# Performance work log

Measured on AMD Instinct MI355X. Metric: run time of the kernel, lower is better.

Reference implementation:

```python
import jax, jax.numpy as jnp
import numpy as np

B, D, R, E, L = 16384, 1024, 64, 4, 3


def setup_inputs() -> dict:
    key = jax.random.key(0)
    ks = jax.random.split(key, 6)
    x0 = jax.random.normal(ks[0], (B, D), dtype=jnp.float32)
    # Expert low-rank factors: U projects D->R, V projects R->D (both bias-free)
    U = jax.random.normal(ks[1], (L, E, D, R), dtype=jnp.float32) * (1.0 / np.sqrt(D))
    V = jax.random.normal(ks[2], (L, E, R, D), dtype=jnp.float32) * (1.0 / np.sqrt(R))
    # Gate Linear(D, E) with bias
    gW = jax.random.normal(ks[3], (L, D, E), dtype=jnp.float32) * (1.0 / np.sqrt(D))
    gb = jax.random.normal(ks[4], (L, E), dtype=jnp.float32) * 0.01
    # Per-layer bias added after mixing (initialized zeros in torch; small random here)
    bias = jax.random.normal(ks[5], (L, D), dtype=jnp.float32) * 0.01
    return {"x0": x0, "U": U, "V": V, "gW": gW, "gb": gb, "bias": bias}


def reference(x0, U, V, gW, gb, bias):
    x = x0
    for l in range(L):
        # batched low-rank expert MLPs: [B,D] -> [B,E,R] -> relu -> [B,E,D]
        h = jax.nn.relu(jnp.einsum('bd,edr->ber', x, U[l]))
        expert_out = jnp.einsum('ber,erd->bed', h, V[l])
        # soft gate over experts
        gate = jax.nn.softmax(x @ gW[l] + gb[l], axis=-1)  # [B,E]
        mixed = jnp.einsum('be,bed->bd', gate, expert_out)  # [B,D]
        x = x0 * mixed + bias[l] + x
    return x
```

## Files before the change

kernel.cpp:

```cpp
#include <hip/hip_runtime.h>

#define DEVI __device__ __forceinline__

typedef __bf16 bf16x8 __attribute__((ext_vector_type(8)));
typedef float f32x4 __attribute__((ext_vector_type(4)));
typedef unsigned short u16x8 __attribute__((ext_vector_type(8)));

DEVI unsigned short f2bf(float f) {
  unsigned u = __builtin_bit_cast(unsigned, f);
  u += 0x7FFFu + ((u >> 16) & 1u);
  return (unsigned short)(u >> 16);
}
DEVI float bf2f(unsigned short h) {
  return __builtin_bit_cast(float, (unsigned)h << 16);
}


__global__ __launch_bounds__(256) void cast_x0_kernel(const float* __restrict__ x,
                                                      unsigned short* __restrict__ xb) {
  int i = blockIdx.x * 256 + threadIdx.x;
  const f32x4* p = (const f32x4*)x;
  f32x4 a = p[2 * i], b = p[2 * i + 1];
  u16x8 o;
  o[0] = f2bf(a[0]); o[1] = f2bf(a[1]); o[2] = f2bf(a[2]); o[3] = f2bf(a[3]);
  o[4] = f2bf(b[0]); o[5] = f2bf(b[1]); o[6] = f2bf(b[2]); o[7] = f2bf(b[3]);
  ((u16x8*)xb)[i] = o;
}

__global__ __launch_bounds__(256) void pack_w1_kernel(const float* __restrict__ U,
                                                      unsigned short* __restrict__ W1T) {
  int idx = blockIdx.x * 256 + threadIdx.x;
  int l = idx >> 18;
  int rem = idx & 262143;
  int n = rem >> 10, k = rem & 1023;
  int e = n >> 6, r = n & 63;
  W1T[idx] = f2bf(U[(size_t)(((l * 4 + e) << 10) + k) * 64 + r]);
}

__global__ __launch_bounds__(256) void pack_v2_kernel(const float* __restrict__ V,
                                                      unsigned short* __restrict__ V2T) {
  int idx = blockIdx.x * 256 + threadIdx.x;
  int l = idx >> 18;
  int rem = idx & 262143;
  int d = rem >> 8, c = rem & 255;
  int e = c >> 6, r = c & 63;
  V2T[idx] = f2bf(V[(size_t)(((l * 4 + e) * 64 + r) << 10) + d]);
}

__global__ __launch_bounds__(256) void pack_gw_kernel(const float* __restrict__ gW,
                                                      unsigned short* __restrict__ gWT) {
  int idx = blockIdx.x * 256 + threadIdx.x;
  int l = idx >> 14;
  int n = (idx >> 10) & 15;
  int k = idx & 1023;
  float v = (n < 4) ? gW[l * 4096 + k * 4 + n] : 0.0f;
  gWT[idx] = f2bf(v);
}

__global__ __launch_bounds__(256) void k1_kernel(const unsigned short* __restrict__ A,
                                                 const unsigned short* __restrict__ Bw,
                                                 const unsigned short* __restrict__ gWT,
                                                 const float* __restrict__ gb,
                                                 unsigned short* __restrict__ Hg) {
  constexpr int K = 1024;
  __shared__ char lds[20480];
  __shared__ float gls[128];
  int t = threadIdx.x;
  int wid = t >> 6, lane = t & 63;
  int g4 = lane >> 4, l15 = lane & 15;
  int wm = wid >> 1, wn = wid & 1;

  int j = blockIdx.x;
  int s = j >> 3;
  int p = (j & 7) * 64 + (s >> 1);
  int ybl = s & 1;
  int m0 = p * 32, n0 = ybl * 128;

  int srow = t >> 3;
  int scolb = ((t & 7) * 16) ^ ((srow & 7) << 4);
  const unsigned short* Asrc = A + (size_t)(m0 + srow) * K + (scolb >> 1);
  const unsigned short* Bsrc = Bw + (size_t)(n0 + srow) * K + (scolb >> 1);

  f32x4 acc[4], accg;
  {
    f32x4 z = {0.f, 0.f, 0.f, 0.f};
    accg = z;
#pragma unroll
    for (int n = 0; n < 4; ++n) acc[n] = z;
  }

  for (int ks = 0; ks < K; ks += 64) {
    __syncthreads();
    __builtin_amdgcn_global_load_lds(
        (const __attribute__((address_space(1))) void*)(Asrc + ks),
        (__attribute__((address_space(3))) void*)(lds + wid * 1024), 16, 0, 0);
#pragma unroll
    for (int i = 0; i < 4; ++i)
      __builtin_amdgcn_global_load_lds(
          (const __attribute__((address_space(1))) void*)(Bsrc + (size_t)i * 32 * K + ks),
          (__attribute__((address_space(3))) void*)(lds + 4096 + i * 4096 + wid * 1024), 16, 0, 0);
    __syncthreads();
#pragma unroll
    for (int kk = 0; kk < 2; ++kk) {
      bf16x8 af;
      {
        int row = wm * 16 + l15;
        af = *(const bf16x8*)(lds + row * 128 + ((kk * 64 + g4 * 16) ^ ((row & 7) << 4)));
      }
      bf16x8 gf;
      if (wn == 0) gf = *(const bf16x8*)(gWT + (size_t)l15 * 1024 + ks + kk * 32 + g4 * 8);
#pragma unroll
      for (int n = 0; n < 4; ++n) {
        int row = wn * 64 + n * 16 + l15;
        bf16x8 bfr = *(const bf16x8*)(lds + 4096 + row * 128 +
                                      ((kk * 64 + g4 * 16) ^ ((row & 7) << 4)));
        acc[n] = __builtin_amdgcn_mfma_f32_16x16x32_bf16(af, bfr, acc[n], 0, 0, 0);
      }
      if (wn == 0)
        accg = __builtin_amdgcn_mfma_f32_16x16x32_bf16(af, gf, accg, 0, 0, 0);
    }
  }

  if (wn == 0) {
    float gbv = gb[l15 & 3];
#pragma unroll
    for (int jj = 0; jj < 4; ++jj) {
      float v = accg[jj] + gbv;
      float mx = fmaxf(v, __shfl_xor(v, 1));
      mx = fmaxf(mx, __shfl_xor(mx, 2));
      float ev = __expf(v - mx);
      float sm = ev + __shfl_xor(ev, 1);
      sm += __shfl_xor(sm, 2);
      if (l15 < 4) gls[(wm * 16 + g4 * 4 + jj) * 4 + l15] = ev / sm;
    }
  }
  __syncthreads();

  int e = ybl * 2 + wn;
#pragma unroll
  for (int n = 0; n < 4; ++n) {
#pragma unroll
    for (int jj = 0; jj < 4; ++jj) {
      int row = wm * 16 + g4 * 4 + jj;
      int col = wn * 64 + n * 16 + l15;
      float v = fmaxf(acc[n][jj], 0.f) * gls[row * 4 + e];
      *(unsigned short*)(lds + 4096 + row * 256 + ((col * 2) ^ ((row & 7) << 4))) = f2bf(v);
    }
  }
  __syncthreads();

#pragma unroll
  for (int i = 0; i < 2; ++i) {
    int row = i * 16 + (t >> 4);
    int seg = (t & 15) * 16;
    u16x8 v = *(const u16x8*)(lds + 4096 + row * 256 + (seg ^ ((row & 7) << 4)));
    *(u16x8*)(Hg + (size_t)(m0 + row) * 256 + n0 + (seg >> 1)) = v;
  }
}

__global__ __launch_bounds__(256) void k2_kernel(const unsigned short* __restrict__ A,
                                                 const unsigned short* __restrict__ Bw,
                                                 const unsigned short* __restrict__ x0b,
                                                 const float* __restrict__ x0f,
                                                 const unsigned short* __restrict__ xcur,
                                                 const float* __restrict__ biasl,
                                                 unsigned short* __restrict__ xnext,
                                                 float* __restrict__ out,
                                                 int last, int use_x0b) {
  constexpr int K = 256;
  __shared__ char lds[24576];
  int t = threadIdx.x;
  int wid = t >> 6, lane = t & 63;
  int g4 = lane >> 4, l15 = lane & 15;
  int wm = wid >> 1, wn = wid & 1;

  int j = blockIdx.x;
  int s = j >> 3;
  int xbl = (j & 7) * 32 + (s >> 3);
  int ybl = s & 7;
  int m0 = xbl * 64, n0 = ybl * 128;

  int srow = t >> 3;
  int scolb = ((t & 7) * 16) ^ ((srow & 7) << 4);
  const unsigned short* Asrc = A + (size_t)(m0 + srow) * K + (scolb >> 1);
  const unsigned short* Bsrc = Bw + (size_t)(n0 + srow) * K + (scolb >> 1);

  f32x4 acc[2][4];
#pragma unroll
  for (int m = 0; m < 2; ++m)
#pragma unroll
    for (int n = 0; n < 4; ++n) { f32x4 z = {0.f, 0.f, 0.f, 0.f}; acc[m][n] = z; }

  for (int ks = 0; ks < K; ks += 64) {
    __syncthreads();
#pragma unroll
    for (int i = 0; i < 2; ++i)
      __builtin_amdgcn_global_load_lds(
          (const __attribute__((address_space(1))) void*)(Asrc + (size_t)i * 32 * K + ks),
          (__attribute__((address_space(3))) void*)(lds + i * 4096 + wid * 1024), 16, 0, 0);
#pragma unroll
    for (int i = 0; i < 4; ++i)
      __builtin_amdgcn_global_load_lds(
          (const __attribute__((address_space(1))) void*)(Bsrc + (size_t)i * 32 * K + ks),
          (__attribute__((address_space(3))) void*)(lds + 8192 + i * 4096 + wid * 1024), 16, 0, 0);
    __syncthreads();
#pragma unroll
    for (int kk = 0; kk < 2; ++kk) {
      bf16x8 af[2];
#pragma unroll
      for (int m = 0; m < 2; ++m) {
        int row = wm * 32 + m * 16 + l15;
        af[m] = *(const bf16x8*)(lds + row * 128 + ((kk * 64 + g4 * 16) ^ ((row & 7) << 4)));
      }
#pragma unroll
      for (int n = 0; n < 4; ++n) {
        int row = wn * 64 + n * 16 + l15;
        bf16x8 bfr = *(const bf16x8*)(lds + 8192 + row * 128 +
                                      ((kk * 64 + g4 * 16) ^ ((row & 7) << 4)));
#pragma unroll
        for (int m = 0; m < 2; ++m)
          acc[m][n] = __builtin_amdgcn_mfma_f32_16x16x32_bf16(af[m], bfr, acc[m][n], 0, 0, 0);
      }
    }
  }
  __syncthreads();

#pragma unroll
  for (int m = 0; m < 2; ++m) {
#pragma unroll
    for (int n = 0; n < 4; ++n) {
#pragma unroll
      for (int jj = 0; jj < 4; ++jj) {
        int row = wm * 32 + m * 16 + g4 * 4 + jj;
        int col = wn * 64 + n * 16 + l15;
        *(unsigned short*)(lds + 8192 + row * 256 + ((col * 2) ^ ((row & 7) << 4))) =
            f2bf(acc[m][n][jj]);
      }
    }
  }
  __syncthreads();

#pragma unroll
  for (int i = 0; i < 4; ++i) {
    int row = i * 16 + (t >> 4);
    int seg = (t & 15) * 16;
    u16x8 a8 = *(const u16x8*)(lds + 8192 + row * 256 + (seg ^ ((row & 7) << 4)));
    size_t goff = (size_t)(m0 + row) * 1024 + n0 + (seg >> 1);
    u16x8 cv = *(const u16x8*)(xcur + goff);
    float x0v[8];
    if (use_x0b) {
      u16x8 xv = *(const u16x8*)(x0b + goff);
#pragma unroll
      for (int k = 0; k < 8; ++k) x0v[k] = bf2f(xv[k]);
    } else {
      f32x4 xa = *(const f32x4*)(x0f + goff);
      f32x4 xb2 = *(const f32x4*)(x0f + goff + 4);
#pragma unroll
      for (int k = 0; k < 4; ++k) { x0v[k] = xa[k]; x0v[k + 4] = xb2[k]; }
    }
    const float* bp = biasl + n0 + (seg >> 1);
    f32x4 b0 = *(const f32x4*)bp;
    f32x4 b1 = *(const f32x4*)(bp + 4);
    float r[8];
#pragma unroll
    for (int k = 0; k < 8; ++k) {
      float bv = (k < 4) ? b0[k & 3] : b1[k & 3];
      r[k] = x0v[k] * bf2f(a8[k]) + bv + bf2f(cv[k]);
    }
    if (last) {
      f32x4 r0, r1;
#pragma unroll
      for (int k = 0; k < 4; ++k) { r0[k] = r[k]; r1[k] = r[k + 4]; }
      *(f32x4*)(out + goff) = r0;
      *(f32x4*)(out + goff + 4) = r1;
    } else {
      u16x8 o;
#pragma unroll
      for (int k = 0; k < 8; ++k) o[k] = f2bf(r[k]);
      *(u16x8*)(xnext + goff) = o;
    }
  }
}

extern "C" void kernel_launch(void* const* d_in, const int* in_sizes, int n_in,
                              void* d_out, int out_size, void* d_ws, size_t ws_size,
                              hipStream_t stream) {
  const float* x0 = (const float*)d_in[0];
  const float* U = (const float*)d_in[1];
  const float* V = (const float*)d_in[2];
  const float* gW = (const float*)d_in[3];
  const float* gb = (const float*)d_in[4];
  const float* bias = (const float*)d_in[5];
  float* out = (float*)d_out;
  char* ws = (char*)d_ws;

  const size_t SZ_X = 33554432;
  const size_t SZ_HG = 8388608;
  const size_t SZ_W = 1572864;
  const size_t SZ_GW = 98304;
  bool use_x0b = ws_size >= (2 * SZ_X + SZ_HG + 2 * SZ_W + SZ_GW);

  size_t off = 0;
  unsigned short* x0b = nullptr;
  if (use_x0b) { x0b = (unsigned short*)(ws + off); off += SZ_X; }
  unsigned short* xbf = (unsigned short*)(ws + off); off += SZ_X;
  unsigned short* hg = (unsigned short*)(ws + off); off += SZ_HG;
  unsigned short* W1T = (unsigned short*)(ws + off); off += SZ_W;
  unsigned short* V2T = (unsigned short*)(ws + off); off += SZ_W;
  unsigned short* gWT = (unsigned short*)(ws + off); off += SZ_GW;

  unsigned short* xinit = use_x0b ? x0b : xbf;

  cast_x0_kernel<<<8192, 256, 0, stream>>>(x0, xinit);
  pack_w1_kernel<<<3072, 256, 0, stream>>>(U, W1T);
  pack_v2_kernel<<<3072, 256, 0, stream>>>(V, V2T);
  pack_gw_kernel<<<192, 256, 0, stream>>>(gW, gWT);

  for (int l = 0; l < 3; ++l) {
    const unsigned short* xs = (l == 0) ? xinit : xbf;
    k1_kernel<<<1024, 256, 0, stream>>>(xs, W1T + l * 262144, gWT + l * 16384,
                                        gb + l * 4, hg);
    k2_kernel<<<2048, 256, 0, stream>>>(hg, V2T + l * 262144,
                                        use_x0b ? x0b : nullptr, x0, xs,
                                        bias + l * 1024, xbf, out,
                                        (l == 2) ? 1 : 0, use_x0b ? 1 : 0);
  }
}
```

Baseline: 178.4 us.

## Double K-step to 128 in both GEMMs and halve k2 M-tile to 32 rows

Both GEMM kernels now stage 128-wide K slices per iteration, which halves the number of barrier-separated load/compute rounds and doubles LDS use to 40 KB. k2 also shrinks its M tile from 64 to 32 rows and doubles its grid to 4096 blocks, giving more blocks but less reuse of each B tile per block. The larger LDS footprint may lower occupancy, and the smaller k2 tile increases total weight traffic from L2.

```diff
diff --git a/kernel.cpp b/kernel.cpp
--- a/kernel.cpp
+++ b/kernel.cpp
@@ -63,7 +63,7 @@
                                                  const float* __restrict__ gb,
                                                  unsigned short* __restrict__ Hg) {
   constexpr int K = 1024;
-  __shared__ char lds[20480];
+  __shared__ char lds[40960];
   __shared__ float gls[128];
   int t = threadIdx.x;
   int wid = t >> 6, lane = t & 63;
@@ -76,8 +76,8 @@
   int ybl = s & 1;
   int m0 = p * 32, n0 = ybl * 128;
 
-  int srow = t >> 3;
-  int scolb = ((t & 7) * 16) ^ ((srow & 7) << 4);
+  int srow = t >> 4;
+  int scolb = ((t & 15) * 16) ^ ((srow & 7) << 4);
   const unsigned short* Asrc = A + (size_t)(m0 + srow) * K + (scolb >> 1);
   const unsigned short* Bsrc = Bw + (size_t)(n0 + srow) * K + (scolb >> 1);
 
@@ -89,31 +89,33 @@
     for (int n = 0; n < 4; ++n) acc[n] = z;
   }
 
-  for (int ks = 0; ks < K; ks += 64) {
+  for (int ks = 0; ks < K; ks += 128) {
     __syncthreads();
-    __builtin_amdgcn_global_load_lds(
-        (const __attribute__((address_space(1))) void*)(Asrc + ks),
-        (__attribute__((address_space(3))) void*)(lds + wid * 1024), 16, 0, 0);
-#pragma unroll
-    for (int i = 0; i < 4; ++i)
+#pragma unroll
+    for (int i = 0; i < 2; ++i)
       __builtin_amdgcn_global_load_lds(
-          (const __attribute__((address_space(1))) void*)(Bsrc + (size_t)i * 32 * K + ks),
-          (__attribute__((address_space(3))) void*)(lds + 4096 + i * 4096 + wid * 1024), 16, 0, 0);
+          (const __attribute__((address_space(1))) void*)(Asrc + (size_t)i * 16 * K + ks),
+          (__attribute__((address_space(3))) void*)(lds + i * 4096 + wid * 1024), 16, 0, 0);
+#pragma unroll
+    for (int i = 0; i < 8; ++i)
+      __builtin_amdgcn_global_load_lds(
+          (const __attribute__((address_space(1))) void*)(Bsrc + (size_t)i * 16 * K + ks),
+          (__attribute__((address_space(3))) void*)(lds + 8192 + i * 4096 + wid * 1024), 16, 0, 0);
     __syncthreads();
 #pragma unroll
-    for (int kk = 0; kk < 2; ++kk) {
+    for (int kk = 0; kk < 4; ++kk) {
+      int kkb = kk * 64 + g4 * 16;
       bf16x8 af;
       {
         int row = wm * 16 + l15;
-        af = *(const bf16x8*)(lds + row * 128 + ((kk * 64 + g4 * 16) ^ ((row & 7) << 4)));
+        af = *(const bf16x8*)(lds + row * 256 + (kkb ^ ((row & 7) << 4)));
       }
       bf16x8 gf;
       if (wn == 0) gf = *(const bf16x8*)(gWT + (size_t)l15 * 1024 + ks + kk * 32 + g4 * 8);
 #pragma unroll
       for (int n = 0; n < 4; ++n) {
         int row = wn * 64 + n * 16 + l15;
-        bf16x8 bfr = *(const bf16x8*)(lds + 4096 + row * 128 +
-                                      ((kk * 64 + g4 * 16) ^ ((row & 7) << 4)));
+        bf16x8 bfr = *(const bf16x8*)(lds + 8192 + row * 256 + (kkb ^ ((row & 7) << 4)));
         acc[n] = __builtin_amdgcn_mfma_f32_16x16x32_bf16(af, bfr, acc[n], 0, 0, 0);
       }
       if (wn == 0)
@@ -144,7 +146,7 @@
       int row = wm * 16 + g4 * 4 + jj;
       int col = wn * 64 + n * 16 + l15;
       float v = fmaxf(acc[n][jj], 0.f) * gls[row * 4 + e];
-      *(unsigned short*)(lds + 4096 + row * 256 + ((col * 2) ^ ((row & 7) << 4))) = f2bf(v);
+      *(unsigned short*)(lds + 8192 + row * 256 + ((col * 2) ^ ((row & 7) << 4))) = f2bf(v);
     }
   }
   __syncthreads();
@@ -153,7 +155,7 @@
   for (int i = 0; i < 2; ++i) {
     int row = i * 16 + (t >> 4);
     int seg = (t & 15) * 16;
-    u16x8 v = *(const u16x8*)(lds + 4096 + row * 256 + (seg ^ ((row & 7) << 4)));
+    u16x8 v = *(const u16x8*)(lds + 8192 + row * 256 + (seg ^ ((row & 7) << 4)));
     *(u16x8*)(Hg + (size_t)(m0 + row) * 256 + n0 + (seg >> 1)) = v;
   }
 }
@@ -168,7 +170,7 @@
                                                  float* __restrict__ out,
                                                  int last, int use_x0b) {
   constexpr int K = 256;
-  __shared__ char lds[24576];
+  __shared__ char lds[40960];
   int t = threadIdx.x;
   int wid = t >> 6, lane = t & 63;
   int g4 = lane >> 4, l15 = lane & 15;
@@ -176,72 +178,64 @@
 
   int j = blockIdx.x;
   int s = j >> 3;
-  int xbl = (j & 7) * 32 + (s >> 3);
+  int xbl = (j & 7) * 64 + (s >> 3);
   int ybl = s & 7;
-  int m0 = xbl * 64, n0 = ybl * 128;
-
-  int srow = t >> 3;
-  int scolb = ((t & 7) * 16) ^ ((srow & 7) << 4);
+  int m0 = xbl * 32, n0 = ybl * 128;
+
+  int srow = t >> 4;
+  int scolb = ((t & 15) * 16) ^ ((srow & 7) << 4);
   const unsigned short* Asrc = A + (size_t)(m0 + srow) * K + (scolb >> 1);
   const unsigned short* Bsrc = Bw + (size_t)(n0 + srow) * K + (scolb >> 1);
 
-  f32x4 acc[2][4];
-#pragma unroll
-  for (int m = 0; m < 2; ++m)
-#pragma unroll
-    for (int n = 0; n < 4; ++n) { f32x4 z = {0.f, 0.f, 0.f, 0.f}; acc[m][n] = z; }
-
-  for (int ks = 0; ks < K; ks += 64) {
+  f32x4 acc[4];
+#pragma unroll
+  for (int n = 0; n < 4; ++n) { f32x4 z = {0.f, 0.f, 0.f, 0.f}; acc[n] = z; }
+
+  for (int ks = 0; ks < K; ks += 128) {
     __syncthreads();
 #pragma unroll
     for (int i = 0; i < 2; ++i)
       __builtin_amdgcn_global_load_lds(
-          (const __attribute__((address_space(1))) void*)(Asrc + (size_t)i * 32 * K + ks),
+          (const __attribute__((address_space(1))) void*)(Asrc + (size_t)i * 16 * K + ks),
           (__attribute__((address_space(3))) void*)(lds + i * 4096 + wid * 1024), 16, 0, 0);
 #pragma unroll
-    for (int i = 0; i < 4; ++i)
+    for (int i = 0; i < 8; ++i)
       __builtin_amdgcn_global_load_lds(
-          (const __attribute__((address_space(1))) void*)(Bsrc + (size_t)i * 32 * K + ks),
+          (const __attribute__((address_space(1))) void*)(Bsrc + (size_t)i * 16 * K + ks),
           (__attribute__((address_space(3))) void*)(lds + 8192 + i * 4096 + wid * 1024), 16, 0, 0);
     __syncthreads();
 #pragma unroll
-    for (int kk = 0; kk < 2; ++kk) {
-      bf16x8 af[2];
-#pragma unroll
-      for (int m = 0; m < 2; ++m) {
-        int row = wm * 32 + m * 16 + l15;
-        af[m] = *(const bf16x8*)(lds + row * 128 + ((kk * 64 + g4 * 16) ^ ((row & 7) << 4)));
+    for (int kk = 0; kk < 4; ++kk) {
+      int kkb = kk * 64 + g4 * 16;
+      bf16x8 af;
+      {
+        int row = wm * 16 + l15;
+        af = *(const bf16x8*)(lds + row * 256 + (kkb ^ ((row & 7) << 4)));
       }
 #pragma unroll
       for (int n = 0; n < 4; ++n) {
         int row = wn * 64 + n * 16 + l15;
-        bf16x8 bfr = *(const bf16x8*)(lds + 8192 + row * 128 +
-                                      ((kk * 64 + g4 * 16) ^ ((row & 7) << 4)));
-#pragma unroll
-        for (int m = 0; m < 2; ++m)
-          acc[m][n] = __builtin_amdgcn_mfma_f32_16x16x32_bf16(af[m], bfr, acc[m][n], 0, 0, 0);
+        bf16x8 bfr = *(const bf16x8*)(lds + 8192 + row * 256 + (kkb ^ ((row & 7) << 4)));
+        acc[n] = __builtin_amdgcn_mfma_f32_16x16x32_bf16(af, bfr, acc[n], 0, 0, 0);
       }
     }
   }
   __syncthreads();
 
 #pragma unroll
-  for (int m = 0; m < 2; ++m) {
-#pragma unroll
-    for (int n = 0; n < 4; ++n) {
-#pragma unroll
-      for (int jj = 0; jj < 4; ++jj) {
-        int row = wm * 32 + m * 16 + g4 * 4 + jj;
-        int col = wn * 64 + n * 16 + l15;
-        *(unsigned short*)(lds + 8192 + row * 256 + ((col * 2) ^ ((row & 7) << 4))) =
-            f2bf(acc[m][n][jj]);
-      }
+  for (int n = 0; n < 4; ++n) {
+#pragma unroll
+    for (int jj = 0; jj < 4; ++jj) {
+      int row = wm * 16 + g4 * 4 + jj;
+      int col = wn * 64 + n * 16 + l15;
+      *(unsigned short*)(lds + 8192 + row * 256 + ((col * 2) ^ ((row & 7) << 4))) =
+          f2bf(acc[n][jj]);
     }
   }
   __syncthreads();
 
 #pragma unroll
-  for (int i = 0; i < 4; ++i) {
+  for (int i = 0; i < 2; ++i) {
     int row = i * 16 + (t >> 4);
     int seg = (t & 15) * 16;
     u16x8 a8 = *(const u16x8*)(lds + 8192 + row * 256 + (seg ^ ((row & 7) << 4)));
@@ -320,7 +314,7 @@
     const unsigned short* xs = (l == 0) ? xinit : xbf;
     k1_kernel<<<1024, 256, 0, stream>>>(xs, W1T + l * 262144, gWT + l * 16384,
                                         gb + l * 4, hg);
-    k2_kernel<<<2048, 256, 0, stream>>>(hg, V2T + l * 262144,
+    k2_kernel<<<4096, 256, 0, stream>>>(hg, V2T + l * 262144,
                                         use_x0b ? x0b : nullptr, x0, xs,
                                         bias + l * 1024, xbf, out,
                                         (l == 2) ? 1 : 0, use_x0b ? 1 : 0);
```

After: 209.0 us. 1.17x slower.

## Double-buffer k1 LDS tiles to overlap global loads with MFMA compute

Applied to the files above, without the earlier changes.

Doubles the k1 kernel's LDS buffer so the next K-slice is fetched with global_load_lds while the current slice feeds the MFMAs. Synchronisation moves from __syncthreads pairs to explicit vmcnt waits plus s_barrier. The gate-weight fragments are now loaded ahead of each stage, and all waves compute the gate MFMA instead of only wn==0, which adds redundant MFMA work. Doubling LDS per block may reduce occupancy.

```diff
diff --git a/kernel.cpp b/kernel.cpp
--- a/kernel.cpp
+++ b/kernel.cpp
@@ -63,7 +63,7 @@
                                                  const float* __restrict__ gb,
                                                  unsigned short* __restrict__ Hg) {
   constexpr int K = 1024;
-  __shared__ char lds[20480];
+  __shared__ char lds[40960];
   __shared__ float gls[128];
   int t = threadIdx.x;
   int wid = t >> 6, lane = t & 63;
@@ -71,15 +71,16 @@
   int wm = wid >> 1, wn = wid & 1;
 
   int j = blockIdx.x;
-  int s = j >> 3;
-  int p = (j & 7) * 64 + (s >> 1);
-  int ybl = s & 1;
+  int sj = j >> 3;
+  int p = (j & 7) * 64 + (sj >> 1);
+  int ybl = sj & 1;
   int m0 = p * 32, n0 = ybl * 128;
 
   int srow = t >> 3;
   int scolb = ((t & 7) * 16) ^ ((srow & 7) << 4);
   const unsigned short* Asrc = A + (size_t)(m0 + srow) * K + (scolb >> 1);
   const unsigned short* Bsrc = Bw + (size_t)(n0 + srow) * K + (scolb >> 1);
+  const unsigned short* gsrc = gWT + (size_t)l15 * 1024 + g4 * 8;
 
   f32x4 acc[4], accg;
   {
@@ -89,37 +90,50 @@
     for (int n = 0; n < 4; ++n) acc[n] = z;
   }
 
-  for (int ks = 0; ks < K; ks += 64) {
-    __syncthreads();
-    __builtin_amdgcn_global_load_lds(
-        (const __attribute__((address_space(1))) void*)(Asrc + ks),
-        (__attribute__((address_space(3))) void*)(lds + wid * 1024), 16, 0, 0);
-#pragma unroll
-    for (int i = 0; i < 4; ++i)
-      __builtin_amdgcn_global_load_lds(
-          (const __attribute__((address_space(1))) void*)(Bsrc + (size_t)i * 32 * K + ks),
-          (__attribute__((address_space(3))) void*)(lds + 4096 + i * 4096 + wid * 1024), 16, 0, 0);
-    __syncthreads();
+#define K1_STAGE(b, ks)                                                                       \
+  {                                                                                           \
+    __builtin_amdgcn_global_load_lds(                                                         \
+        (const __attribute__((address_space(1))) void*)(Asrc + (ks)),                         \
+        (__attribute__((address_space(3))) void*)(lds + (b) * 20480 + wid * 1024), 16, 0, 0); \
+    _Pragma("unroll") for (int i = 0; i < 4; ++i) __builtin_amdgcn_global_load_lds(           \
+        (const __attribute__((address_space(1))) void*)(Bsrc + (size_t)i * 32 * K + (ks)),    \
+        (__attribute__((address_space(3))) void*)(lds + (b) * 20480 + 4096 + i * 4096 +       \
+                                                  wid * 1024),                                \
+        16, 0, 0);                                                                            \
+  }
+
+  K1_STAGE(0, 0);
+
+  for (int s = 0; s < 16; ++s) {
+    bf16x8 gf0 = *(const bf16x8*)(gsrc + s * 64);
+    bf16x8 gf1 = *(const bf16x8*)(gsrc + s * 64 + 32);
+    if (s < 15) {
+      K1_STAGE((s + 1) & 1, (s + 1) * 64);
+      asm volatile("s_waitcnt vmcnt(5)" ::: "memory");
+    } else {
+      asm volatile("s_waitcnt vmcnt(0)" ::: "memory");
+    }
+    __builtin_amdgcn_s_barrier();
+    const char* base = lds + (s & 1) * 20480;
 #pragma unroll
     for (int kk = 0; kk < 2; ++kk) {
       bf16x8 af;
       {
         int row = wm * 16 + l15;
-        af = *(const bf16x8*)(lds + row * 128 + ((kk * 64 + g4 * 16) ^ ((row & 7) << 4)));
-      }
-      bf16x8 gf;
-      if (wn == 0) gf = *(const bf16x8*)(gWT + (size_t)l15 * 1024 + ks + kk * 32 + g4 * 8);
+        af = *(const bf16x8*)(base + row * 128 + ((kk * 64 + g4 * 16) ^ ((row & 7) << 4)));
+      }
 #pragma unroll
       for (int n = 0; n < 4; ++n) {
         int row = wn * 64 + n * 16 + l15;
-        bf16x8 bfr = *(const bf16x8*)(lds + 4096 + row * 128 +
+        bf16x8 bfr = *(const bf16x8*)(base + 4096 + row * 128 +
                                       ((kk * 64 + g4 * 16) ^ ((row & 7) << 4)));
         acc[n] = __builtin_amdgcn_mfma_f32_16x16x32_bf16(af, bfr, acc[n], 0, 0, 0);
       }
-      if (wn == 0)
-        accg = __builtin_amdgcn_mfma_f32_16x16x32_bf16(af, gf, accg, 0, 0, 0);
-    }
-  }
+      accg = __builtin_amdgcn_mfma_f32_16x16x32_bf16(af, kk ? gf1 : gf0, accg, 0, 0, 0);
+    }
+    __builtin_amdgcn_s_barrier();
+  }
+#undef K1_STAGE
 
   if (wn == 0) {
     float gbv = gb[l15 & 3];
```

Measured after the change: 204.9 us. 1.15x slower.
